# Kernel optimization log

Hardware: AMD Instinct MI355X
Metric: run time of the kernel (lower is better)

## Reference

```python
import jax, jax.numpy as jnp
import numpy as np

NUM_CODES = 1024
DIM = 256


def setup_inputs() -> dict:
    key = jax.random.key(0)
    k1, k2 = jax.random.split(key)
    x = jax.random.normal(k1, (16, 256, 4096), dtype=jnp.float32)
    # torch init: uniform(-1/num_codes, 1/num_codes)
    codebook = jax.random.uniform(k2, (NUM_CODES, DIM), dtype=jnp.float32,
                                  minval=-1.0 / NUM_CODES, maxval=1.0 / NUM_CODES)
    return {"x": x, "codebook": codebook}


def reference(x, codebook):
    # x: [B, C, T], codebook: [K, C]
    B, C, T = x.shape
    flat = jnp.transpose(x, (0, 2, 1)).reshape(-1, C)  # [N, C], N = B*T
    # squared L2 distances: |f|^2 - 2 f.e + |e|^2
    dist = (jnp.sum(flat * flat, axis=1, keepdims=True)
            - 2.0 * jnp.einsum('nc,kc->nk', flat, codebook)
            + jnp.sum(codebook * codebook, axis=1))  # [N, K]
    encode_idx = jnp.argmin(dist, axis=1)  # [N]
    quant = codebook[encode_idx].reshape(B, T, C).transpose(0, 2, 1)  # [B, C, T]
    # dual MSE loss (codebook + commitment, both weight 1)
    loss = (jnp.mean((jax.lax.stop_gradient(quant) - x) ** 2)
            + jnp.mean((quant - jax.lax.stop_gradient(x)) ** 2))
    # straight-through estimator
    quantized = x + jax.lax.stop_gradient(quant - x)
    return quantized, loss
```

## Files before the change

### kernel.cpp

```cpp
#include <hip/hip_runtime.h>

#define DIM 256
#define T_LEN 4096
#define K_CODES 1024
#define N_TOK 65536
#define NELEM 16777216


typedef __attribute__((ext_vector_type(8))) short bf16x8;
typedef __attribute__((ext_vector_type(16))) float f32x16;
typedef __attribute__((ext_vector_type(8))) int i32x8;

__device__ __forceinline__ unsigned short f2bf(float f) {
    unsigned u = __builtin_bit_cast(unsigned, f);
    return (unsigned short)((u + 0x7FFFu + ((u >> 16) & 1u)) >> 16);
}
__device__ __forceinline__ float bf2f(unsigned short h) {
    return __builtin_bit_cast(float, (unsigned)h << 16);
}
__device__ __forceinline__ unsigned f2u(float f) { return __builtin_bit_cast(unsigned, f); }
__device__ __forceinline__ float u2f(unsigned u) { return __builtin_bit_cast(float, u); }
__device__ __forceinline__ unsigned umin2(unsigned a, unsigned b) { return a < b ? a : b; }

union FragU { bf16x8 v; unsigned short u[8]; };

#define GLLOAD(gsrc, lbase)                                                              \
    __builtin_amdgcn_global_load_lds(                                                    \
        (const __attribute__((address_space(1))) unsigned int*)(gsrc),                   \
        (__attribute__((address_space(3))) unsigned int*)(lbase), 16, 0, 0)

__device__ __forceinline__ unsigned cvt8n(float a, float b) {
    unsigned r;
    asm("v_cvt_pk_fp8_f32 %0, -%1, -%2" : "=v"(r) : "v"(a), "v"(b));
    return r;
}
__device__ __forceinline__ unsigned cvt8(float a, float b) {
    unsigned r;
    asm("v_cvt_pk_fp8_f32 %0, %1, %2" : "=v"(r) : "v"(a), "v"(b));
    return r;
}

__global__ __launch_bounds__(256) void prep(const float* __restrict__ cb,
                                            char* __restrict__ cbb8,
                                            unsigned* __restrict__ cnh2) {
    const int k = blockIdx.x * 4 + (threadIdx.x >> 6);
    const int lane = threadIdx.x & 63;
    float4 v = *reinterpret_cast<const float4*>(cb + (size_t)k * DIM + lane * 4);
    float s = v.x * v.x + v.y * v.y + v.z * v.z + v.w * v.w;
    #pragma unroll
    for (int off = 32; off; off >>= 1) s += __shfl_down(s, off);
    if (lane == 0) {
        float cn = 128.0f + 128.0f * s;
        unsigned short chi = f2bf(cn);
        unsigned short clo = f2bf(cn - bf2f(chi));
        cnh2[k] = (unsigned)chi | ((unsigned)clo << 16);
    }
    const unsigned wlo = cvt8(256.0f * v.x, 256.0f * v.y);
    const unsigned whi = cvt8(256.0f * v.z, 256.0f * v.w);
    const unsigned dw = __builtin_amdgcn_perm(whi, wlo, 0x05040100u);
    const int d0 = lane * 4;
    const int wnd = d0 >> 6, dwi = d0 & 63, hs = dwi >> 5, i = dwi & 31;
    const int byte = (k >> 5) * 8192 + wnd * 2048 + hs * 1024 + (i >> 4) * 512
                   + (k & 31) * 16 + (i & 15);
    *reinterpret_cast<unsigned*>(cbb8 + byte) = dw;
}

__global__ __launch_bounds__(256, 4) void vq_fused(const float* __restrict__ x,
                                                   const char* __restrict__ cbb8,
                                                   const unsigned* __restrict__ cnh2,
                                                   const float* __restrict__ cbf,
                                                   float* __restrict__ out,
                                                   float* __restrict__ part) {
    __shared__ __align__(16) char ring[32768];
    __shared__ unsigned cnl[1024];
    __shared__ unsigned kbx[4][32];
    __shared__ int kkl[64];
    __shared__ float wsum[4];
    const int tid = threadIdx.x;
    const int w = tid >> 6, lane = tid & 63, hi = lane >> 5, ln31 = lane & 31;
    const int tg = w >> 1, kh = w & 1;
    const int tw0 = blockIdx.x * 64;
    const int b = tw0 >> 12, tb = tw0 & (T_LEN - 1);

    cnl[tid] = cnh2[tid];
    cnl[tid + 256] = cnh2[tid + 256];
    cnl[tid + 512] = cnh2[tid + 512];
    cnl[tid + 768] = cnh2[tid + 768];

    const int tqi = tid & 15, cqi = tid >> 4;
    const float* xb = x + (size_t)b * DIM * T_LEN + tb + 4 * tqi;
    float x2s = 0.0f;
    #pragma unroll
    for (int ii = 0; ii < 4; ++ii) {
        const int cl = (ii * 16 + cqi) * 4;
        const float* p = xb + (size_t)cl * T_LEN;
        const float4 P0 = *reinterpret_cast<const float4*>(p);
        const float4 P1 = *reinterpret_cast<const float4*>(p + T_LEN);
        const float4 P2 = *reinterpret_cast<const float4*>(p + 2 * T_LEN);
        const float4 P3 = *reinterpret_cast<const float4*>(p + 3 * T_LEN);
        x2s = fmaf(P0.x, P0.x, fmaf(P0.y, P0.y, fmaf(P0.z, P0.z, fmaf(P0.w, P0.w, x2s))));
        x2s = fmaf(P1.x, P1.x, fmaf(P1.y, P1.y, fmaf(P1.z, P1.z, fmaf(P1.w, P1.w, x2s))));
        x2s = fmaf(P2.x, P2.x, fmaf(P2.y, P2.y, fmaf(P2.z, P2.z, fmaf(P2.w, P2.w, x2s))));
        x2s = fmaf(P3.x, P3.x, fmaf(P3.y, P3.y, fmaf(P3.z, P3.z, fmaf(P3.w, P3.w, x2s))));
        const unsigned lo0 = cvt8n(P0.x, P0.y), hi0 = cvt8n(P0.z, P0.w);
        const unsigned lo1 = cvt8n(P1.x, P1.y), hi1 = cvt8n(P1.z, P1.w);
        const unsigned lo2 = cvt8n(P2.x, P2.y), hi2 = cvt8n(P2.z, P2.w);
        const unsigned lo3 = cvt8n(P3.x, P3.y), hi3 = cvt8n(P3.z, P3.w);
        const unsigned s01 = __builtin_amdgcn_perm(lo1, lo0, 0x05010400u);
        const unsigned s23 = __builtin_amdgcn_perm(lo3, lo2, 0x05010400u);
        const unsigned u01 = __builtin_amdgcn_perm(hi1, hi0, 0x05010400u);
        const unsigned u23 = __builtin_amdgcn_perm(hi3, hi2, 0x05010400u);
        const unsigned t0 = __builtin_amdgcn_perm(s23, s01, 0x05040100u);
        const unsigned t1 = __builtin_amdgcn_perm(s23, s01, 0x07060302u);
        const unsigned t2 = __builtin_amdgcn_perm(u23, u01, 0x05040100u);
        const unsigned t3 = __builtin_amdgcn_perm(u23, u01, 0x07060302u);
        const int ta = 4 * tqi;
        *reinterpret_cast<unsigned*>(ring + (ta + 0) * 256 + (cl ^ (((ta + 0) & 15) << 3))) = t0;
        *reinterpret_cast<unsigned*>(ring + (ta + 1) * 256 + (cl ^ (((ta + 1) & 15) << 3))) = t1;
        *reinterpret_cast<unsigned*>(ring + (ta + 2) * 256 + (cl ^ (((ta + 2) & 15) << 3))) = t2;
        *reinterpret_cast<unsigned*>(ring + (ta + 3) * 256 + (cl ^ (((ta + 3) & 15) << 3))) = t3;
    }
    __syncthreads();

    i32x8 xf0[4];
    {
        const int tp0 = tg * 32 + ln31;
        const int z0 = (tp0 & 15) << 3;
        #pragma unroll
        for (int wnd = 0; wnd < 4; ++wnd) {
            #pragma unroll
            for (int g = 0; g < 4; ++g) {
                const int o = wnd * 64 + hi * 32 + g * 8;
                const long v0 = *reinterpret_cast<const long*>(ring + tp0 * 256 + (o ^ z0));
                xf0[wnd][2 * g] = (int)(unsigned)(v0 & 0xFFFFFFFFu);
                xf0[wnd][2 * g + 1] = (int)(unsigned)(((unsigned long)v0) >> 32);
            }
        }
    }
    __syncthreads();

    auto stage = [&](int kc, int buf) {
        char* lb = ring + buf * 16384 + w * 1024;
        const char* gc = cbb8 + kc * 8192;
        #pragma unroll
        for (int j = 0; j < 4; ++j) {
            const int o = j * 4096 + tid * 16;
            GLLOAD(gc + (o & 8191) + (o >> 13) * 131072, lb + j * 4096);
        }
    };
    stage(0, 0);

    FragU cfr0, onef;
    #pragma unroll
    for (int i = 0; i < 8; ++i) onef.u[i] = (hi == 0 && i < 2) ? 0x3F80 : 0;

    unsigned b0a = 0xFFFFFFFFu, b0b = 0xFFFFFFFFu;

    for (int kc = 0; kc < 16; ++kc) {
        const int cur = kc & 1;
        if (kc < 15) {
            stage(kc + 1, cur ^ 1);
            asm volatile("s_waitcnt vmcnt(4)" ::: "memory");
        } else {
            asm volatile("s_waitcnt vmcnt(0)" ::: "memory");
        }
        __builtin_amdgcn_s_barrier();
        __builtin_amdgcn_sched_barrier(0);

        const unsigned d = cnl[kh * 512 + kc * 32 + ln31];
        #pragma unroll
        for (int i = 0; i < 8; ++i) cfr0.u[i] = 0;
        if (hi == 0) {
            cfr0.u[0] = (unsigned short)(d & 0xFFFFu);
            cfr0.u[1] = (unsigned short)(d >> 16);
        }

        f32x16 acc0;
        #pragma unroll
        for (int i = 0; i < 16; ++i) acc0[i] = 0.0f;
        acc0 = __builtin_amdgcn_mfma_f32_32x32x16_bf16(cfr0.v, onef.v, acc0, 0, 0, 0);

        const char* cbpA = ring + cur * 16384 + kh * 8192 + hi * 1024 + ln31 * 16;
        #pragma unroll
        for (int wnd = 0; wnd < 4; ++wnd) {
            const uint4 alo = *reinterpret_cast<const uint4*>(cbpA + wnd * 2048);
            const uint4 ahi = *reinterpret_cast<const uint4*>(cbpA + wnd * 2048 + 512);
            i32x8 aw;
            aw[0] = (int)alo.x; aw[1] = (int)alo.y; aw[2] = (int)alo.z; aw[3] = (int)alo.w;
            aw[4] = (int)ahi.x; aw[5] = (int)ahi.y; aw[6] = (int)ahi.z; aw[7] = (int)ahi.w;
            acc0 = __builtin_amdgcn_mfma_scale_f32_32x32x64_f8f6f4(
                aw, xf0[wnd], acc0, 0, 0, 0, 0x7F7F7F7F, 0, 0x7F7F7F7F);
        }

        const int kbl = kh * 512 + kc * 32 + hi * 4;
        #pragma unroll
        for (int rg = 0; rg < 16; ++rg) {
            const unsigned kk = (unsigned)(kbl + (rg & 3) + 8 * (rg >> 2));
            const unsigned p0 = (f2u(acc0[rg]) & 0xFFFFFC00u) | kk;
            if (rg & 1) b0b = umin2(b0b, p0);
            else        b0a = umin2(b0a, p0);
        }
        __builtin_amdgcn_s_barrier();
        __builtin_amdgcn_sched_barrier(0);
    }

    unsigned best0 = umin2(b0a, b0b);
    best0 = umin2(best0, __shfl_xor(best0, 32));
    if (hi == 0) kbx[w][ln31] = best0;
    __syncthreads();

    float red = x2s;
    if (tid < 64) {
        const int tgn = tid >> 5, t32 = tid & 31;
        const unsigned key = umin2(kbx[tgn * 2][t32], kbx[tgn * 2 + 1][t32]);
        kkl[tid] = (int)(key & 1023u);
        red += (u2f(key & 0xFFFFFC00u) - 128.0f) * 0.0078125f;
    }
    #pragma unroll
    for (int off = 32; off; off >>= 1) red += __shfl_down(red, off);
    if (lane == 0) wsum[w] = red;
    __syncthreads();
    if (tid == 0) part[blockIdx.x] = wsum[0] + wsum[1] + wsum[2] + wsum[3];

    float* fs = (float*)ring;
    const int tt = tid & 63, ch = tid >> 6;
    const size_t rowb = (size_t)kkl[tt] * DIM;
    #pragma unroll 1
    for (int sl = 0; sl < 8; ++sl) {
        float4 g0 = *reinterpret_cast<const float4*>(cbf + rowb + sl * 32 + ch * 8);
        float4 g1 = *reinterpret_cast<const float4*>(cbf + rowb + sl * 32 + ch * 8 + 4);
        __syncthreads();
        const int c0 = ch * 8;
        fs[(c0 + 0) * 68 + tt] = g0.x;
        fs[(c0 + 1) * 68 + tt] = g0.y;
        fs[(c0 + 2) * 68 + tt] = g0.z;
        fs[(c0 + 3) * 68 + tt] = g0.w;
        fs[(c0 + 4) * 68 + tt] = g1.x;
        fs[(c0 + 5) * 68 + tt] = g1.y;
        fs[(c0 + 6) * 68 + tt] = g1.z;
        fs[(c0 + 7) * 68 + tt] = g1.w;
        __syncthreads();
        #pragma unroll
        for (int p = 0; p < 2; ++p) {
            const int c = tid >> 3, tq = (tid & 7) + p * 8;
            const float4 v = *reinterpret_cast<const float4*>(fs + c * 68 + tq * 4);
            *reinterpret_cast<float4*>(
                out + (((size_t)(b * DIM + sl * 32 + c)) << 12) + tb + tq * 4) = v;
        }
    }
}

__global__ __launch_bounds__(256) void finalize(const float* __restrict__ part,
                                                float* __restrict__ loss_out) {
    double s = (double)part[threadIdx.x] + (double)part[threadIdx.x + 256]
             + (double)part[threadIdx.x + 512] + (double)part[threadIdx.x + 768];
    #pragma unroll
    for (int off = 32; off; off >>= 1) s += __shfl_down(s, off);
    __shared__ double wsum[4];
    const int lane = threadIdx.x & 63, wv = threadIdx.x >> 6;
    if (lane == 0) wsum[wv] = s;
    __syncthreads();
    if (threadIdx.x == 0)
        *loss_out = (float)(2.0 * (wsum[0] + wsum[1] + wsum[2] + wsum[3]) / (double)NELEM);
}

extern "C" void kernel_launch(void* const* d_in, const int* in_sizes, int n_in,
                              void* d_out, int out_size, void* d_ws, size_t ws_size,
                              hipStream_t stream) {
    const float* x  = (const float*)d_in[0];
    const float* cb = (const float*)d_in[1];
    float* out = (float*)d_out;
    unsigned* ws = (unsigned*)d_ws;
    unsigned* cnh2 = ws;
    float* part = (float*)(ws + 1024);
    char* cbb8 = (char*)(ws + 4096);

    prep<<<K_CODES / 4, 256, 0, stream>>>(cb, cbb8, cnh2);
    vq_fused<<<N_TOK / 64, 256, 0, stream>>>(x, cbb8, cnh2, cb, out, part);
    finalize<<<1, 256, 0, stream>>>(part, out + NELEM);
}
```

Measured before the change: 50.89 us.

## Process two token tiles per block, overlapping ingest and gather with MFMA loops

After: 53.47 us. +5.1%, slower.

```diff
diff --git a/kernel.cpp b/kernel.cpp
--- a/kernel.cpp
+++ b/kernel.cpp
@@ -65,21 +65,22 @@
     *reinterpret_cast<unsigned*>(cbb8 + byte) = dw;
 }
 
-__global__ __launch_bounds__(256, 4) void vq_fused(const float* __restrict__ x,
+__global__ __launch_bounds__(256, 2) void vq_fused(const float* __restrict__ x,
                                                    const char* __restrict__ cbb8,
                                                    const unsigned* __restrict__ cnh2,
                                                    const float* __restrict__ cbf,
                                                    float* __restrict__ out,
                                                    float* __restrict__ part) {
     __shared__ __align__(16) char ring[32768];
+    __shared__ __align__(16) char xbuf[16384];
     __shared__ unsigned cnl[1024];
     __shared__ unsigned kbx[4][32];
-    __shared__ int kkl[64];
+    __shared__ int kklA[64], kklB[64];
     __shared__ float wsum[4];
     const int tid = threadIdx.x;
     const int w = tid >> 6, lane = tid & 63, hi = lane >> 5, ln31 = lane & 31;
     const int tg = w >> 1, kh = w & 1;
-    const int tw0 = blockIdx.x * 64;
+    const int tw0 = blockIdx.x * 128;
     const int b = tw0 >> 12, tb = tw0 & (T_LEN - 1);
 
     cnl[tid] = cnh2[tid];
@@ -88,24 +89,26 @@
     cnl[tid + 768] = cnh2[tid + 768];
 
     const int tqi = tid & 15, cqi = tid >> 4;
-    const float* xb = x + (size_t)b * DIM * T_LEN + tb + 4 * tqi;
     float x2s = 0.0f;
-    #pragma unroll
-    for (int ii = 0; ii < 4; ++ii) {
+
+    auto ing_load = [&](const float* xbase, int ii, float4* P) {
         const int cl = (ii * 16 + cqi) * 4;
-        const float* p = xb + (size_t)cl * T_LEN;
-        const float4 P0 = *reinterpret_cast<const float4*>(p);
-        const float4 P1 = *reinterpret_cast<const float4*>(p + T_LEN);
-        const float4 P2 = *reinterpret_cast<const float4*>(p + 2 * T_LEN);
-        const float4 P3 = *reinterpret_cast<const float4*>(p + 3 * T_LEN);
-        x2s = fmaf(P0.x, P0.x, fmaf(P0.y, P0.y, fmaf(P0.z, P0.z, fmaf(P0.w, P0.w, x2s))));
-        x2s = fmaf(P1.x, P1.x, fmaf(P1.y, P1.y, fmaf(P1.z, P1.z, fmaf(P1.w, P1.w, x2s))));
-        x2s = fmaf(P2.x, P2.x, fmaf(P2.y, P2.y, fmaf(P2.z, P2.z, fmaf(P2.w, P2.w, x2s))));
-        x2s = fmaf(P3.x, P3.x, fmaf(P3.y, P3.y, fmaf(P3.z, P3.z, fmaf(P3.w, P3.w, x2s))));
-        const unsigned lo0 = cvt8n(P0.x, P0.y), hi0 = cvt8n(P0.z, P0.w);
-        const unsigned lo1 = cvt8n(P1.x, P1.y), hi1 = cvt8n(P1.z, P1.w);
-        const unsigned lo2 = cvt8n(P2.x, P2.y), hi2 = cvt8n(P2.z, P2.w);
-        const unsigned lo3 = cvt8n(P3.x, P3.y), hi3 = cvt8n(P3.z, P3.w);
+        const float* p = xbase + (size_t)cl * T_LEN;
+        P[0] = *reinterpret_cast<const float4*>(p);
+        P[1] = *reinterpret_cast<const float4*>(p + T_LEN);
+        P[2] = *reinterpret_cast<const float4*>(p + 2 * T_LEN);
+        P[3] = *reinterpret_cast<const float4*>(p + 3 * T_LEN);
+    };
+    auto ing_proc = [&](int ii, const float4* P, char* lds) {
+        const int cl = (ii * 16 + cqi) * 4;
+        x2s = fmaf(P[0].x, P[0].x, fmaf(P[0].y, P[0].y, fmaf(P[0].z, P[0].z, fmaf(P[0].w, P[0].w, x2s))));
+        x2s = fmaf(P[1].x, P[1].x, fmaf(P[1].y, P[1].y, fmaf(P[1].z, P[1].z, fmaf(P[1].w, P[1].w, x2s))));
+        x2s = fmaf(P[2].x, P[2].x, fmaf(P[2].y, P[2].y, fmaf(P[2].z, P[2].z, fmaf(P[2].w, P[2].w, x2s))));
+        x2s = fmaf(P[3].x, P[3].x, fmaf(P[3].y, P[3].y, fmaf(P[3].z, P[3].z, fmaf(P[3].w, P[3].w, x2s))));
+        const unsigned lo0 = cvt8n(P[0].x, P[0].y), hi0 = cvt8n(P[0].z, P[0].w);
+        const unsigned lo1 = cvt8n(P[1].x, P[1].y), hi1 = cvt8n(P[1].z, P[1].w);
+        const unsigned lo2 = cvt8n(P[2].x, P[2].y), hi2 = cvt8n(P[2].z, P[2].w);
+        const unsigned lo3 = cvt8n(P[3].x, P[3].y), hi3 = cvt8n(P[3].z, P[3].w);
         const unsigned s01 = __builtin_amdgcn_perm(lo1, lo0, 0x05010400u);
         const unsigned s23 = __builtin_amdgcn_perm(lo3, lo2, 0x05010400u);
         const unsigned u01 = __builtin_amdgcn_perm(hi1, hi0, 0x05010400u);
@@ -115,15 +118,12 @@
         const unsigned t2 = __builtin_amdgcn_perm(u23, u01, 0x05040100u);
         const unsigned t3 = __builtin_amdgcn_perm(u23, u01, 0x07060302u);
         const int ta = 4 * tqi;
-        *reinterpret_cast<unsigned*>(ring + (ta + 0) * 256 + (cl ^ (((ta + 0) & 15) << 3))) = t0;
-        *reinterpret_cast<unsigned*>(ring + (ta + 1) * 256 + (cl ^ (((ta + 1) & 15) << 3))) = t1;
-        *reinterpret_cast<unsigned*>(ring + (ta + 2) * 256 + (cl ^ (((ta + 2) & 15) << 3))) = t2;
-        *reinterpret_cast<unsigned*>(ring + (ta + 3) * 256 + (cl ^ (((ta + 3) & 15) << 3))) = t3;
-    }
-    __syncthreads();
-
-    i32x8 xf0[4];
-    {
+        *reinterpret_cast<unsigned*>(lds + (ta + 0) * 256 + (cl ^ (((ta + 0) & 15) << 3))) = t0;
+        *reinterpret_cast<unsigned*>(lds + (ta + 1) * 256 + (cl ^ (((ta + 1) & 15) << 3))) = t1;
+        *reinterpret_cast<unsigned*>(lds + (ta + 2) * 256 + (cl ^ (((ta + 2) & 15) << 3))) = t2;
+        *reinterpret_cast<unsigned*>(lds + (ta + 3) * 256 + (cl ^ (((ta + 3) & 15) << 3))) = t3;
+    };
+    auto read_frags = [&](const char* src, i32x8* xf) {
         const int tp0 = tg * 32 + ln31;
         const int z0 = (tp0 & 15) << 3;
         #pragma unroll
@@ -131,14 +131,12 @@
             #pragma unroll
             for (int g = 0; g < 4; ++g) {
                 const int o = wnd * 64 + hi * 32 + g * 8;
-                const long v0 = *reinterpret_cast<const long*>(ring + tp0 * 256 + (o ^ z0));
-                xf0[wnd][2 * g] = (int)(unsigned)(v0 & 0xFFFFFFFFu);
-                xf0[wnd][2 * g + 1] = (int)(unsigned)(((unsigned long)v0) >> 32);
+                const long v0 = *reinterpret_cast<const long*>(src + tp0 * 256 + (o ^ z0));
+                xf[wnd][2 * g] = (int)(unsigned)(v0 & 0xFFFFFFFFu);
+                xf[wnd][2 * g + 1] = (int)(unsigned)(((unsigned long)v0) >> 32);
             }
         }
-    }
-    __syncthreads();
-
+    };
     auto stage = [&](int kc, int buf) {
         char* lb = ring + buf * 16384 + w * 1024;
         const char* gc = cbb8 + kc * 8192;
@@ -148,38 +146,24 @@
             GLLOAD(gc + (o & 8191) + (o >> 13) * 131072, lb + j * 4096);
         }
     };
-    stage(0, 0);
-
-    FragU cfr0, onef;
+
+    FragU onef;
     #pragma unroll
     for (int i = 0; i < 8; ++i) onef.u[i] = (hi == 0 && i < 2) ? 0x3F80 : 0;
 
-    unsigned b0a = 0xFFFFFFFFu, b0b = 0xFFFFFFFFu;
-
-    for (int kc = 0; kc < 16; ++kc) {
-        const int cur = kc & 1;
-        if (kc < 15) {
-            stage(kc + 1, cur ^ 1);
-            asm volatile("s_waitcnt vmcnt(4)" ::: "memory");
-        } else {
-            asm volatile("s_waitcnt vmcnt(0)" ::: "memory");
-        }
-        __builtin_amdgcn_s_barrier();
-        __builtin_amdgcn_sched_barrier(0);
-
+    auto mfma_round = [&](const i32x8* xf, int cur, int kc, unsigned& ba, unsigned& bb) {
         const unsigned d = cnl[kh * 512 + kc * 32 + ln31];
+        FragU cfr0;
         #pragma unroll
         for (int i = 0; i < 8; ++i) cfr0.u[i] = 0;
         if (hi == 0) {
             cfr0.u[0] = (unsigned short)(d & 0xFFFFu);
             cfr0.u[1] = (unsigned short)(d >> 16);
         }
-
         f32x16 acc0;
         #pragma unroll
         for (int i = 0; i < 16; ++i) acc0[i] = 0.0f;
         acc0 = __builtin_amdgcn_mfma_f32_32x32x16_bf16(cfr0.v, onef.v, acc0, 0, 0, 0);
-
         const char* cbpA = ring + cur * 16384 + kh * 8192 + hi * 1024 + ln31 * 16;
         #pragma unroll
         for (int wnd = 0; wnd < 4; ++wnd) {
@@ -189,71 +173,179 @@
             aw[0] = (int)alo.x; aw[1] = (int)alo.y; aw[2] = (int)alo.z; aw[3] = (int)alo.w;
             aw[4] = (int)ahi.x; aw[5] = (int)ahi.y; aw[6] = (int)ahi.z; aw[7] = (int)ahi.w;
             acc0 = __builtin_amdgcn_mfma_scale_f32_32x32x64_f8f6f4(
-                aw, xf0[wnd], acc0, 0, 0, 0, 0x7F7F7F7F, 0, 0x7F7F7F7F);
-        }
-
+                aw, xf[wnd], acc0, 0, 0, 0, 0x7F7F7F7F, 0, 0x7F7F7F7F);
+        }
         const int kbl = kh * 512 + kc * 32 + hi * 4;
         #pragma unroll
         for (int rg = 0; rg < 16; ++rg) {
             const unsigned kk = (unsigned)(kbl + (rg & 3) + 8 * (rg >> 2));
             const unsigned p0 = (f2u(acc0[rg]) & 0xFFFFFC00u) | kk;
-            if (rg & 1) b0b = umin2(b0b, p0);
-            else        b0a = umin2(b0a, p0);
+            if (rg & 1) bb = umin2(bb, p0);
+            else        ba = umin2(ba, p0);
+        }
+    };
+
+    const float* xbA = x + (size_t)b * DIM * T_LEN + tb + 4 * tqi;
+    const float* xbB = xbA + 64;
+
+    #pragma unroll
+    for (int ii = 0; ii < 4; ++ii) {
+        float4 P[4];
+        ing_load(xbA, ii, P);
+        ing_proc(ii, P, ring);
+    }
+    __syncthreads();
+    i32x8 xfA[4];
+    read_frags(ring, xfA);
+    __syncthreads();
+
+    stage(0, 0);
+    unsigned a0 = 0xFFFFFFFFu, a1 = 0xFFFFFFFFu;
+
+    for (int kc = 0; kc < 16; ++kc) {
+        const int cur = kc & 1;
+        float4 PB[4];
+        const bool ing = (kc < 4);
+        if (kc < 15) {
+            if (ing) ing_load(xbB, kc, PB);
+            __builtin_amdgcn_sched_barrier(0);
+            stage(kc + 1, cur ^ 1);
+            if (ing) asm volatile("s_waitcnt vmcnt(8)" ::: "memory");
+            else     asm volatile("s_waitcnt vmcnt(4)" ::: "memory");
+        } else {
+            asm volatile("s_waitcnt vmcnt(0)" ::: "memory");
         }
         __builtin_amdgcn_s_barrier();
         __builtin_amdgcn_sched_barrier(0);
-    }
-
-    unsigned best0 = umin2(b0a, b0b);
-    best0 = umin2(best0, __shfl_xor(best0, 32));
-    if (hi == 0) kbx[w][ln31] = best0;
-    __syncthreads();
-
-    float red = x2s;
+        mfma_round(xfA, cur, kc, a0, a1);
+        __builtin_amdgcn_sched_barrier(0);
+        if (ing) ing_proc(kc, PB, xbuf);
+        __builtin_amdgcn_s_barrier();
+        __builtin_amdgcn_sched_barrier(0);
+    }
+
+    unsigned bestA = umin2(a0, a1);
+    bestA = umin2(bestA, __shfl_xor(bestA, 32));
+    if (hi == 0) kbx[w][ln31] = bestA;
+    __syncthreads();
     if (tid < 64) {
         const int tgn = tid >> 5, t32 = tid & 31;
         const unsigned key = umin2(kbx[tgn * 2][t32], kbx[tgn * 2 + 1][t32]);
-        kkl[tid] = (int)(key & 1023u);
-        red += (u2f(key & 0xFFFFFC00u) - 128.0f) * 0.0078125f;
-    }
+        kklA[tid] = (int)(key & 1023u);
+        x2s += (u2f(key & 0xFFFFFC00u) - 128.0f) * 0.0078125f;
+    }
+    i32x8 xfB[4];
+    read_frags(xbuf, xfB);
+    __syncthreads();
+    const int ttS = tid & 63, chS = tid >> 6;
+    const size_t rowbA = (size_t)kklA[ttS] * DIM;
+    float* fs = (float*)xbuf;
+
+    stage(0, 0);
+    unsigned c0 = 0xFFFFFFFFu, c1 = 0xFFFFFFFFu;
+    float4 G0 = {0, 0, 0, 0}, G1 = {0, 0, 0, 0};
+
+    for (int kc = 0; kc < 16; ++kc) {
+        const int cur = kc & 1;
+        if (kc < 15) {
+            stage(kc + 1, cur ^ 1);
+            if (kc == 0)      { asm volatile("s_waitcnt vmcnt(4)" ::: "memory"); }
+            else if (kc == 1) { asm volatile("s_waitcnt vmcnt(6)" ::: "memory"); }
+            else if (kc & 1)  { asm volatile("s_waitcnt vmcnt(8)" ::: "memory"); }
+            else              { asm volatile("s_waitcnt vmcnt(4)" ::: "memory"); }
+        } else {
+            asm volatile("s_waitcnt vmcnt(0)" ::: "memory");
+        }
+        __builtin_amdgcn_s_barrier();
+        __builtin_amdgcn_sched_barrier(0);
+        if (kc & 1) {
+            const int c0i = chS * 8;
+            fs[(c0i + 0) * 68 + ttS] = G0.x;
+            fs[(c0i + 1) * 68 + ttS] = G0.y;
+            fs[(c0i + 2) * 68 + ttS] = G0.z;
+            fs[(c0i + 3) * 68 + ttS] = G0.w;
+            fs[(c0i + 4) * 68 + ttS] = G1.x;
+            fs[(c0i + 5) * 68 + ttS] = G1.y;
+            fs[(c0i + 6) * 68 + ttS] = G1.z;
+            fs[(c0i + 7) * 68 + ttS] = G1.w;
+        } else if (kc >= 2) {
+            const int sl = (kc - 2) >> 1;
+            #pragma unroll
+            for (int p = 0; p < 2; ++p) {
+                const int c = tid >> 3, tq = (tid & 7) + p * 8;
+                const float4 v = *reinterpret_cast<const float4*>(fs + c * 68 + tq * 4);
+                *reinterpret_cast<float4*>(
+                    out + (((size_t)(b * DIM + sl * 32 + c)) << 12) + tb + tq * 4) = v;
+            }
+        }
+        __builtin_amdgcn_sched_barrier(0);
+        mfma_round(xfB, cur, kc, c0, c1);
+        __builtin_amdgcn_sched_barrier(0);
+        if (!(kc & 1)) {
+            const int sl = kc >> 1;
+            G0 = *reinterpret_cast<const float4*>(cbf + rowbA + sl * 32 + chS * 8);
+            G1 = *reinterpret_cast<const float4*>(cbf + rowbA + sl * 32 + chS * 8 + 4);
+        }
+        __builtin_amdgcn_s_barrier();
+        __builtin_amdgcn_sched_barrier(0);
+    }
+
+    #pragma unroll
+    for (int p = 0; p < 2; ++p) {
+        const int c = tid >> 3, tq = (tid & 7) + p * 8;
+        const float4 v = *reinterpret_cast<const float4*>(fs + c * 68 + tq * 4);
+        *reinterpret_cast<float4*>(
+            out + (((size_t)(b * DIM + 224 + c)) << 12) + tb + tq * 4) = v;
+    }
+
+    unsigned bestB = umin2(c0, c1);
+    bestB = umin2(bestB, __shfl_xor(bestB, 32));
+    if (hi == 0) kbx[w][ln31] = bestB;
+    __syncthreads();
+    if (tid < 64) {
+        const int tgn = tid >> 5, t32 = tid & 31;
+        const unsigned key = umin2(kbx[tgn * 2][t32], kbx[tgn * 2 + 1][t32]);
+        kklB[tid] = (int)(key & 1023u);
+        x2s += (u2f(key & 0xFFFFFC00u) - 128.0f) * 0.0078125f;
+    }
+    __syncthreads();
+
+    float red = x2s;
     #pragma unroll
     for (int off = 32; off; off >>= 1) red += __shfl_down(red, off);
     if (lane == 0) wsum[w] = red;
     __syncthreads();
     if (tid == 0) part[blockIdx.x] = wsum[0] + wsum[1] + wsum[2] + wsum[3];
 
-    float* fs = (float*)ring;
-    const int tt = tid & 63, ch = tid >> 6;
-    const size_t rowb = (size_t)kkl[tt] * DIM;
+    const size_t rowbB = (size_t)kklB[ttS] * DIM;
     #pragma unroll 1
     for (int sl = 0; sl < 8; ++sl) {
-        float4 g0 = *reinterpret_cast<const float4*>(cbf + rowb + sl * 32 + ch * 8);
-        float4 g1 = *reinterpret_cast<const float4*>(cbf + rowb + sl * 32 + ch * 8 + 4);
+        float4 g0 = *reinterpret_cast<const float4*>(cbf + rowbB + sl * 32 + chS * 8);
+        float4 g1 = *reinterpret_cast<const float4*>(cbf + rowbB + sl * 32 + chS * 8 + 4);
         __syncthreads();
-        const int c0 = ch * 8;
-        fs[(c0 + 0) * 68 + tt] = g0.x;
-        fs[(c0 + 1) * 68 + tt] = g0.y;
-        fs[(c0 + 2) * 68 + tt] = g0.z;
-        fs[(c0 + 3) * 68 + tt] = g0.w;
-        fs[(c0 + 4) * 68 + tt] = g1.x;
-        fs[(c0 + 5) * 68 + tt] = g1.y;
-        fs[(c0 + 6) * 68 + tt] = g1.z;
-        fs[(c0 + 7) * 68 + tt] = g1.w;
+        const int c0i = chS * 8;
+        fs[(c0i + 0) * 68 + ttS] = g0.x;
+        fs[(c0i + 1) * 68 + ttS] = g0.y;
+        fs[(c0i + 2) * 68 + ttS] = g0.z;
+        fs[(c0i + 3) * 68 + ttS] = g0.w;
+        fs[(c0i + 4) * 68 + ttS] = g1.x;
+        fs[(c0i + 5) * 68 + ttS] = g1.y;
+        fs[(c0i + 6) * 68 + ttS] = g1.z;
+        fs[(c0i + 7) * 68 + ttS] = g1.w;
         __syncthreads();
         #pragma unroll
         for (int p = 0; p < 2; ++p) {
             const int c = tid >> 3, tq = (tid & 7) + p * 8;
             const float4 v = *reinterpret_cast<const float4*>(fs + c * 68 + tq * 4);
             *reinterpret_cast<float4*>(
-                out + (((size_t)(b * DIM + sl * 32 + c)) << 12) + tb + tq * 4) = v;
+                out + (((size_t)(b * DIM + sl * 32 + c)) << 12) + tb + 64 + tq * 4) = v;
         }
     }
 }
 
 __global__ __launch_bounds__(256) void finalize(const float* __restrict__ part,
                                                 float* __restrict__ loss_out) {
-    double s = (double)part[threadIdx.x] + (double)part[threadIdx.x + 256]
-             + (double)part[threadIdx.x + 512] + (double)part[threadIdx.x + 768];
+    double s = (double)part[threadIdx.x] + (double)part[threadIdx.x + 256];
     #pragma unroll
     for (int off = 32; off; off >>= 1) s += __shfl_down(s, off);
     __shared__ double wsum[4];
@@ -276,6 +368,6 @@
     char* cbb8 = (char*)(ws + 4096);
 
     prep<<<K_CODES / 4, 256, 0, stream>>>(cb, cbb8, cnh2);
-    vq_fused<<<N_TOK / 64, 256, 0, stream>>>(x, cbb8, cnh2, cb, out, part);
+    vq_fused<<<N_TOK / 128, 256, 0, stream>>>(x, cbb8, cnh2, cb, out, part);
     finalize<<<1, 256, 0, stream>>>(part, out + NELEM);
 }
```
